# Optimization experiments

Hardware: AMD Instinct MI355X
Metric: run time of the kernel (lower is better)

Reference implementation:

```python
import jax, jax.numpy as jnp
import numpy as np
import math

B, T, C, H = 2, 2048, 1024, 16
D = C // H  # head dim = 64


def setup_inputs() -> dict:
    key = jax.random.key(0)
    ks = jax.random.split(key, 9)
    s = 1.0 / math.sqrt(C)
    inp = {
        "x": jax.random.normal(ks[0], (B, T, C), dtype=jnp.float32),
        "Wk": jax.random.normal(ks[1], (C, C), dtype=jnp.float32) * s,
        "bk": jax.random.normal(ks[2], (C,), dtype=jnp.float32) * s,
        "Wq": jax.random.normal(ks[3], (C, C), dtype=jnp.float32) * s,
        "bq": jax.random.normal(ks[4], (C,), dtype=jnp.float32) * s,
        "Wv": jax.random.normal(ks[5], (C, C), dtype=jnp.float32) * s,
        "bv": jax.random.normal(ks[6], (C,), dtype=jnp.float32) * s,
        "Wo": jax.random.normal(ks[7], (C, C), dtype=jnp.float32) * s,
        "bo": jax.random.normal(ks[8], (C,), dtype=jnp.float32) * s,
    }
    return inp


def reference(x, Wk, bk, Wq, bq, Wv, bv, Wo, bo):
    # QKV projections, split heads: [B,T,C] -> [B,H,T,D]
    def proj(W, b):
        return (x @ W.T + b).reshape(B, T, H, D).transpose(0, 2, 1, 3)

    k = proj(Wk, bk)
    q = proj(Wq, bq)
    v = proj(Wv, bv)

    # NOTE: original scales by 1/sqrt(embedding_dim), not head_dim
    scale = 1.0 / math.sqrt(C)
    scores = jnp.einsum("bhtd,bhsd->bhts", q, k) * scale  # [B,H,T,T]
    causal = jnp.tril(jnp.ones((T, T), dtype=bool))
    scores = jnp.where(causal[None, None], scores, -jnp.inf)
    attn = jax.nn.softmax(scores, axis=-1)
    y = jnp.einsum("bhts,bhsd->bhtd", attn, v)  # [B,H,T,D]
    y = y.transpose(0, 2, 1, 3).reshape(B, T, C)
    return y @ Wo.T + bo
```

## Files before the change

### kernel.cpp

```cpp
#include <hip/hip_runtime.h>
#include <hip/hip_bf16.h>
#include <stdint.h>
#include <stddef.h>

#define B_ 2
#define T_ 2048
#define C_ 1024
#define H_ 16
#define D_ 64
#define M_ (B_*T_)

typedef __attribute__((ext_vector_type(8))) short short8;
typedef __attribute__((ext_vector_type(4))) float f32x4;
typedef __attribute__((ext_vector_type(16))) float f32x16;
typedef __attribute__((ext_vector_type(4))) unsigned int u32x4;

__device__ __forceinline__ unsigned short f2bf(float f) {
    unsigned u = __float_as_uint(f);
    unsigned r = 0x7FFFu + ((u >> 16) & 1u);
    return (unsigned short)((u + r) >> 16);
}

__device__ __forceinline__ unsigned cvtpk_bf16(float lo, float hi) {
    unsigned r;
    asm("v_cvt_pk_bf16_f32 %0, %1, %2" : "=v"(r) : "v"(lo), "v"(hi));
    return r;
}

__device__ __forceinline__ float fexp2(float x) {
    float r;
    asm("v_exp_f32 %0, %1" : "=v"(r) : "v"(x));
    return r;
}

__device__ __forceinline__ void plswap(unsigned &a, unsigned &b) {
    asm("v_permlane32_swap_b32 %0, %1" : "+v"(a), "+v"(b));
}

__device__ __forceinline__ float xhalf_max(float v) {
    float a = v, b = v;
    asm("" : "+v"(b));
    asm("v_permlane32_swap_b32 %0, %1" : "+v"(a), "+v"(b));
    return fmaxf(a, b);
}
__device__ __forceinline__ float xhalf_sum(float v) {
    float a = v, b = v;
    asm("" : "+v"(b));
    asm("v_permlane32_swap_b32 %0, %1" : "+v"(a), "+v"(b));
    return a + b;
}

__device__ __forceinline__ void gload16(const void* g, void* l) {
    __builtin_amdgcn_global_load_lds(
        (__attribute__((address_space(1))) void*)g,
        (__attribute__((address_space(3))) void*)l,
        16, 0, 0);
}

__global__ void cvt_bf16(const float* __restrict__ in,
                         unsigned short* __restrict__ out, int n) {
    int idx = (blockIdx.x * blockDim.x + threadIdx.x) * 4;
    if (idx >= n) return;
    float4 v = *reinterpret_cast<const float4*>(in + idx);
    ushort4 o;
    o.x = f2bf(v.x); o.y = f2bf(v.y); o.z = f2bf(v.z); o.w = f2bf(v.w);
    *reinterpret_cast<ushort4*>(out + idx) = o;
}

__global__ void cvt_bf16_w4(const float* __restrict__ a, const float* __restrict__ b,
                            const float* __restrict__ c, const float* __restrict__ d,
                            unsigned short* __restrict__ oa, unsigned short* __restrict__ ob,
                            unsigned short* __restrict__ oc, unsigned short* __restrict__ od,
                            int n) {
    int idx = (blockIdx.x * blockDim.x + threadIdx.x) * 4;
    if (idx >= n) return;
    const float* in = (blockIdx.y == 0) ? a : (blockIdx.y == 1) ? b : (blockIdx.y == 2) ? c : d;
    unsigned short* out = (blockIdx.y == 0) ? oa : (blockIdx.y == 1) ? ob : (blockIdx.y == 2) ? oc : od;
    float4 v = *reinterpret_cast<const float4*>(in + idx);
    ushort4 o;
    o.x = f2bf(v.x); o.y = f2bf(v.y); o.z = f2bf(v.z); o.w = f2bf(v.w);
    *reinterpret_cast<ushort4*>(out + idx) = o;
}

__global__ __launch_bounds__(256) void gemm_qkv(
    const unsigned short* __restrict__ A,
    const unsigned short* __restrict__ W0,
    const unsigned short* __restrict__ W1,
    const unsigned short* __restrict__ W2,
    const float* __restrict__ b0,
    const float* __restrict__ b1,
    const float* __restrict__ b2,
    unsigned short* __restrict__ o0,
    unsigned short* __restrict__ o1,
    unsigned short* __restrict__ o2)
{
    __shared__ unsigned short As[128*32];
    __shared__ unsigned short Bs[128*32];
    int which = blockIdx.x >> 8;
    int bx = blockIdx.x & 255;
    int bm = bx >> 3, bn = bx & 7;
    const unsigned short* W = (which==0) ? W0 : ((which==1) ? W1 : W2);
    const float* bias = (which==0) ? b0 : ((which==1) ? b1 : b2);

    int tid = threadIdx.x;
    int lane = tid & 63;
    int fr = lane & 15, fq = lane >> 4;
    int wid = tid >> 6;
    int wr = wid >> 1, wc = wid & 1;

    int srow = tid >> 2;
    int scol = (tid & 3) << 3;
    const unsigned short* Ab = A + (size_t)(bm*128 + srow) * C_ + scol;
    const unsigned short* Wb = W + (size_t)(bn*128 + srow) * C_ + scol;

    f32x4 acc[4][4] = {};

    for (int kt = 0; kt < C_/32; ++kt) {
        int ko = kt*32;
        gload16(Ab + ko,            &As[tid*8]);
        gload16(Ab + 64*C_ + ko,    &As[2048 + tid*8]);
        gload16(Wb + ko,            &Bs[tid*8]);
        gload16(Wb + 64*C_ + ko,    &Bs[2048 + tid*8]);
        __syncthreads();
        short8 af[4], bfr[4];
        #pragma unroll
        for (int i = 0; i < 4; ++i) {
            af[i]  = *reinterpret_cast<const short8*>(&As[(wr*64 + i*16 + fr)*32 + fq*8]);
            bfr[i] = *reinterpret_cast<const short8*>(&Bs[(wc*64 + i*16 + fr)*32 + fq*8]);
        }
        #pragma unroll
        for (int i = 0; i < 4; ++i)
            #pragma unroll
            for (int j = 0; j < 4; ++j)
                acc[i][j] = __builtin_amdgcn_mfma_f32_16x16x32_bf16(af[i], bfr[j], acc[i][j], 0, 0, 0);
        __syncthreads();
    }

    float sc = (which == 1) ? 0.045084220f : 1.0f;
    int mbase = bm*128 + wr*64;
    int nbase = bn*128 + wc*64;
    #pragma unroll
    for (int j = 0; j < 4; ++j) {
        int col = nbase + j*16 + fr;
        float bv = bias[col];
        int h = col >> 6, d = col & 63;
        #pragma unroll
        for (int i = 0; i < 4; ++i) {
            int r0 = mbase + i*16 + fq*4;
            #pragma unroll
            for (int r = 0; r < 4; ++r) {
                float v = (acc[i][j][r] + bv) * sc;
                int m = r0 + r;
                int b = m >> 11, t = m & (T_-1);
                unsigned short hv = f2bf(v);
                if (which == 2)
                    o2[((size_t)(b*H_ + h)*D_ + d)*T_ + t] = hv;
                else {
                    unsigned short* o = (which==0) ? o0 : o1;
                    o[((size_t)(b*H_ + h)*T_ + t)*D_ + d] = hv;
                }
            }
        }
    }
}

__global__ __launch_bounds__(256) void gemm_out(
    const unsigned short* __restrict__ A,
    const unsigned short* __restrict__ W,
    const float* __restrict__ bias,
    float* __restrict__ out)
{
    __shared__ unsigned short As[128*32];
    __shared__ unsigned short Bs[128*32];
    int bx = blockIdx.x;
    int bm = bx >> 3, bn = bx & 7;

    int tid = threadIdx.x;
    int lane = tid & 63;
    int fr = lane & 15, fq = lane >> 4;
    int wid = tid >> 6;
    int wr = wid >> 1, wc = wid & 1;

    int srow = tid >> 2;
    int scol = (tid & 3) << 3;
    const unsigned short* Ab = A + (size_t)(bm*128 + srow) * C_ + scol;
    const unsigned short* Wb = W + (size_t)(bn*128 + srow) * C_ + scol;

    f32x4 acc[4][4] = {};

    for (int kt = 0; kt < C_/32; ++kt) {
        int ko = kt*32;
        gload16(Ab + ko,            &As[tid*8]);
        gload16(Ab + 64*C_ + ko,    &As[2048 + tid*8]);
        gload16(Wb + ko,            &Bs[tid*8]);
        gload16(Wb + 64*C_ + ko,    &Bs[2048 + tid*8]);
        __syncthreads();
        short8 af[4], bfr[4];
        #pragma unroll
        for (int i = 0; i < 4; ++i) {
            af[i]  = *reinterpret_cast<const short8*>(&As[(wr*64 + i*16 + fr)*32 + fq*8]);
            bfr[i] = *reinterpret_cast<const short8*>(&Bs[(wc*64 + i*16 + fr)*32 + fq*8]);
        }
        #pragma unroll
        for (int i = 0; i < 4; ++i)
            #pragma unroll
            for (int j = 0; j < 4; ++j)
                acc[i][j] = __builtin_amdgcn_mfma_f32_16x16x32_bf16(af[i], bfr[j], acc[i][j], 0, 0, 0);
        __syncthreads();
    }

    int mbase = bm*128 + wr*64;
    int nbase = bn*128 + wc*64;
    #pragma unroll
    for (int j = 0; j < 4; ++j) {
        int col = nbase + j*16 + fr;
        float bv = bias[col];
        #pragma unroll
        for (int i = 0; i < 4; ++i) {
            int r0 = mbase + i*16 + fq*4;
            #pragma unroll
            for (int r = 0; r < 4; ++r)
                out[(size_t)(r0 + r)*C_ + col] = acc[i][j][r] + bv;
        }
    }
}

__device__ __forceinline__ void attn_subtile(
    const short8 (&kf)[4], const short8 (&qf)[4],
    const short8 (&vlo)[2], const short8 (&vhi)[2],
    bool diag, int l31, int hi,
    f32x16& o0, f32x16& o1, float& m_, float& l_)
{
    f32x16 a0 = {};
    __builtin_amdgcn_s_setprio(1);
    a0 = __builtin_amdgcn_mfma_f32_32x32x16_bf16(kf[0], qf[0], a0, 0, 0, 0);
    a0 = __builtin_amdgcn_mfma_f32_32x32x16_bf16(kf[1], qf[1], a0, 0, 0, 0);
    a0 = __builtin_amdgcn_mfma_f32_32x32x16_bf16(kf[2], qf[2], a0, 0, 0, 0);
    a0 = __builtin_amdgcn_mfma_f32_32x32x16_bf16(kf[3], qf[3], a0, 0, 0, 0);
    __builtin_amdgcn_s_setprio(0);

    if (diag) {
        #pragma unroll
        for (int r = 0; r < 16; ++r) {
            int kvl = (r&3) + 8*(r>>2) + 4*hi;
            if (kvl > l31) a0[r] = -1e30f;
        }
    }

    float x0 = fmaxf(a0[0], a0[1]),   x1 = fmaxf(a0[2], a0[3]);
    float x2 = fmaxf(a0[4], a0[5]),   x3 = fmaxf(a0[6], a0[7]);
    float x4 = fmaxf(a0[8], a0[9]),   x5 = fmaxf(a0[10], a0[11]);
    float x6 = fmaxf(a0[12], a0[13]), x7 = fmaxf(a0[14], a0[15]);
    float y0 = fmaxf(x0, x1), y1 = fmaxf(x2, x3), y2 = fmaxf(x4, x5), y3 = fmaxf(x6, x7);
    float pm = fmaxf(fmaxf(y0, y1), fmaxf(y2, y3));
    pm = xhalf_max(pm);

    if (!__all(pm - m_ <= 8.0f)) {
        float mn = fmaxf(m_, pm);
        float alpha = fexp2(m_ - mn);
        l_ *= alpha;
        m_ = mn;
        #pragma unroll
        for (int r = 0; r < 16; ++r) {
            int row = (r&3) + 8*(r>>2) + 4*hi;
            float ar = __shfl(alpha, row);
            o0[r] *= ar;
            o1[r] *= ar;
        }
    }

    #pragma unroll
    for (int r = 0; r < 16; ++r)
        a0[r] = fexp2(a0[r] - m_);
    float s0 = a0[0]+a0[1],  s1 = a0[2]+a0[3],  s2 = a0[4]+a0[5],   s3 = a0[6]+a0[7];
    float s4 = a0[8]+a0[9],  s5 = a0[10]+a0[11], s6 = a0[12]+a0[13], s7 = a0[14]+a0[15];
    float u0 = s0+s1, u1 = s2+s3, u2 = s4+s5, u3 = s6+s7;
    float rs = (u0+u1) + (u2+u3);
    rs = xhalf_sum(rs);
    l_ += rs;

    unsigned pk_[8];
    #pragma unroll
    for (int jj = 0; jj < 8; ++jj)
        pk_[jj] = cvtpk_bf16(a0[2*jj], a0[2*jj+1]);

    #pragma unroll
    for (int kb = 0; kb < 2; ++kb) {
        unsigned fx = pk_[4*kb+0], fz = pk_[4*kb+2];
        unsigned fy = pk_[4*kb+1], fw = pk_[4*kb+3];
        plswap(fx, fz);
        plswap(fy, fw);
        u32x4 wv;
        wv.x = fx; wv.y = fy; wv.z = fz; wv.w = fw;
        short8 pfrag = __builtin_bit_cast(short8, wv);
        __builtin_amdgcn_s_setprio(1);
        o0 = __builtin_amdgcn_mfma_f32_32x32x16_bf16(pfrag, vlo[kb], o0, 0, 0, 0);
        o1 = __builtin_amdgcn_mfma_f32_32x32x16_bf16(pfrag, vhi[kb], o1, 0, 0, 0);
        __builtin_amdgcn_s_setprio(0);
    }
}

__global__ __launch_bounds__(256, 2) void flash_attn(
    const unsigned short* __restrict__ q,
    const unsigned short* __restrict__ k,
    const unsigned short* __restrict__ vt,
    unsigned short* __restrict__ y)
{
    __shared__ __align__(16) unsigned short ST[2][4][4096];
    float* oP  = reinterpret_cast<float*>(&ST[0][0][0]);
    float* mlP = oP + 4*32*68;

    int tid = threadIdx.x, lane = tid & 63, w = tid >> 6;
    int l31 = lane & 31, hi = lane >> 5, rsw = l31 & 7;
    int role = w >> 1, pair = w & 1;
    int bid = blockIdx.x;

    int xcd = bid & 7;
    int r = bid >> 3;
    int bh = xcd*4 + (r & 3);
    int S = 15 - (r >> 2);

    const unsigned short* kp = k  + (size_t)bh*T_*D_;
    const unsigned short* vp = vt + (size_t)bh*D_*T_;

    int rowbase = S*128 + pair*64;
    const unsigned short* qp = q + ((size_t)bh*T_ + rowbase) * D_;

    short8 qf0[4], qf1[4];
    #pragma unroll
    for (int dk = 0; dk < 4; ++dk) {
        qf0[dk] = *reinterpret_cast<const short8*>(qp + (size_t)l31*D_        + dk*16 + hi*8);
        qf1[dk] = *reinterpret_cast<const short8*>(qp + (size_t)(32 + l31)*D_ + dk*16 + hi*8);
    }

    f32x16 o00 = {}, o01 = {}, o10 = {}, o11 = {};
    float m0 = -1e30f, l0 = 0.f, m1 = -1e30f, l1 = 0.f;

    int lim0 = 4*S + 2*pair;
    int lim1 = lim0 + 1;
    int niter = S + 1;

    #define STAGE(ii, bufi)                                                            \
    {                                                                                  \
        _Pragma("unroll")                                                              \
        for (int jj = 0; jj < 2; ++jj) {                                               \
            int c2 = tid + jj*256;                                                     \
            int row_ = c2 >> 3;                                                        \
            int slot_ = (c2 & 7) ^ (row_ & 7);                                         \
            int tl_ = (ii), th_ = S + 1 + (ii);                                        \
            gload16(kp + ((size_t)(tl_*64 + row_))*D_ + slot_*8, &ST[bufi][0][c2*8]);  \
            gload16(kp + ((size_t)(th_*64 + row_))*D_ + slot_*8, &ST[bufi][1][c2*8]);  \
            gload16(vp + (size_t)row_*T_ + tl_*64 + slot_*8,     &ST[bufi][2][c2*8]);  \
            gload16(vp + (size_t)row_*T_ + th_*64 + slot_*8,     &ST[bufi][3][c2*8]);  \
        }                                                                              \
    }

    STAGE(0, 0);
    __syncthreads();

    for (int i = 0; i < niter; ++i) {
        int bufi = i & 1;
        if (i + 1 < niter) STAGE(i + 1, bufi ^ 1);

        const unsigned short* Kl = &ST[bufi][role][0];
        const unsigned short* Vl = &ST[bufi][2 + role][0];
        int t = role ? (S + 1 + i) : i;

        #pragma unroll
        for (int st = 0; st < 2; ++st) {
            int g = 2*t + st;
            if (g <= lim1) {
                short8 kf[4];
                const unsigned short* kr = Kl + (st*32 + l31)*64;
                #pragma unroll
                for (int dk = 0; dk < 4; ++dk)
                    kf[dk] = *reinterpret_cast<const short8*>(kr + (((dk<<1)|hi) ^ rsw)*8);
                short8 vlo[2], vhi[2];
                const unsigned short* vr0 = Vl + l31*64;
                const unsigned short* vr1 = Vl + (32 + l31)*64;
                #pragma unroll
                for (int kb = 0; kb < 2; ++kb) {
                    int sl = (((st<<2) | (kb<<1) | hi) ^ rsw) * 8;
                    vlo[kb] = *reinterpret_cast<const short8*>(vr0 + sl);
                    vhi[kb] = *reinterpret_cast<const short8*>(vr1 + sl);
                }
                if (g <= lim0)
                    attn_subtile(kf, qf0, vlo, vhi, g == lim0, l31, hi, o00, o01, m0, l0);
                attn_subtile(kf, qf1, vlo, vhi, g == lim1, l31, hi, o10, o11, m1, l1);
            }
        }
        __syncthreads();
    }
    #undef STAGE

    if (!role) {
        int s0 = pair*2, s1 = pair*2 + 1;
        #pragma unroll
        for (int rr = 0; rr < 16; ++rr) {
            int crow = (rr&3) + 8*(rr>>2) + 4*hi;
            oP[(s0*32 + crow)*68 + l31]      = o00[rr];
            oP[(s0*32 + crow)*68 + 32 + l31] = o01[rr];
            oP[(s1*32 + crow)*68 + l31]      = o10[rr];
            oP[(s1*32 + crow)*68 + 32 + l31] = o11[rr];
        }
        if (!hi) {
            mlP[s0*32 + l31]       = m0;
            mlP[128 + s0*32 + l31] = l0;
            mlP[s1*32 + l31]       = m1;
            mlP[128 + s1*32 + l31] = l1;
        }
    }
    __syncthreads();
    if (role) {
        int b = bh >> 4, h = bh & 15;
        #pragma unroll
        for (int qq = 0; qq < 2; ++qq) {
            int set = pair*2 + qq;
            const f32x16& po0 = qq ? o10 : o00;
            const f32x16& po1 = qq ? o11 : o01;
            float m_ = qq ? m1 : m0;
            float l_ = qq ? l1 : l0;

            float mA = mlP[set*32 + l31];
            float lA = mlP[128 + set*32 + l31];
            float mN = fmaxf(mA, m_);
            float aA = fexp2(mA - mN);
            float aB = fexp2(m_ - mN);
            float lN = lA*aA + l_*aB;
            float inv = 1.0f / lN;
            float cA = aA * inv, cB = aB * inv;

            #pragma unroll
            for (int rr = 0; rr < 16; ++rr) {
                int crow = (rr&3) + 8*(rr>>2) + 4*hi;
                float cAr = __shfl(cA, crow);
                float cBr = __shfl(cB, crow);
                float vA0 = oP[(set*32 + crow)*68 + l31];
                float vA1 = oP[(set*32 + crow)*68 + 32 + l31];
                int trow = rowbase + qq*32 + crow;
                size_t base = ((size_t)(b*T_ + trow))*C_ + h*64;
                y[base + l31]      = f2bf(vA0*cAr + po0[rr]*cBr);
                y[base + 32 + l31] = f2bf(vA1*cAr + po1[rr]*cBr);
            }
        }
    }
}

extern "C" void kernel_launch(void* const* d_in, const int* in_sizes, int n_in,
                              void* d_out, int out_size, void* d_ws, size_t ws_size,
                              hipStream_t stream) {
    const float* x  = (const float*)d_in[0];
    const float* Wk = (const float*)d_in[1];
    const float* bk = (const float*)d_in[2];
    const float* Wq = (const float*)d_in[3];
    const float* bq = (const float*)d_in[4];
    const float* Wv = (const float*)d_in[5];
    const float* bv = (const float*)d_in[6];
    const float* Wo = (const float*)d_in[7];
    const float* bo = (const float*)d_in[8];
    float* out = (float*)d_out;

    char* ws = (char*)d_ws;
    unsigned short* xb  = (unsigned short*)(ws);
    unsigned short* wkb = (unsigned short*)(ws + ((size_t)8  << 20));
    unsigned short* wqb = (unsigned short*)(ws + ((size_t)10 << 20));
    unsigned short* wvb = (unsigned short*)(ws + ((size_t)12 << 20));
    unsigned short* wob = (unsigned short*)(ws + ((size_t)14 << 20));
    unsigned short* qb  = (unsigned short*)(ws + ((size_t)16 << 20));
    unsigned short* kb  = (unsigned short*)(ws + ((size_t)24 << 20));
    unsigned short* vtb = (unsigned short*)(ws + ((size_t)32 << 20));
    unsigned short* yb  = (unsigned short*)(ws + ((size_t)40 << 20));

    const int nx = B_*T_*C_;
    const int nw = C_*C_;

    cvt_bf16<<<dim3(nx/4/256), dim3(256), 0, stream>>>(x, xb, nx);
    cvt_bf16_w4<<<dim3(nw/4/256, 4), dim3(256), 0, stream>>>(
        Wk, Wq, Wv, Wo, wkb, wqb, wvb, wob, nw);

    gemm_qkv<<<dim3(768), dim3(256), 0, stream>>>(xb, wkb, wqb, wvb, bk, bq, bv, kb, qb, vtb);

    flash_attn<<<dim3(512), dim3(256), 0, stream>>>(qb, kb, vtb, yb);

    gemm_out<<<dim3(256), dim3(256), 0, stream>>>(yb, wob, bo, out);
}
```

Measured before the change: 116.5 us.

## Double GEMM K-tile to 64 with XOR-swizzled LDS and rebalance attention block order

Both projection GEMMs now stage a 64-wide K slice per iteration instead of 32. This halves the number of barrier-separated iterations and doubles the MFMA work done between syncs. The LDS layout uses an XOR swizzle on 16-byte slots to avoid bank conflicts on the fragment reads, at the cost of doubling shared memory per block. The flash attention block-to-tile mapping also changes so the first 256 blocks take the heavy causal tiles in descending order and the second 256 take the light tiles in ascending order, aiming for better load balance.

```diff
diff --git a/kernel.cpp b/kernel.cpp
--- a/kernel.cpp
+++ b/kernel.cpp
@@ -94,8 +94,8 @@
     unsigned short* __restrict__ o1,
     unsigned short* __restrict__ o2)
 {
-    __shared__ unsigned short As[128*32];
-    __shared__ unsigned short Bs[128*32];
+    __shared__ unsigned short As[128*64];
+    __shared__ unsigned short Bs[128*64];
     int which = blockIdx.x >> 8;
     int bx = blockIdx.x & 255;
     int bm = bx >> 3, bn = bx & 7;
@@ -107,32 +107,42 @@
     int fr = lane & 15, fq = lane >> 4;
     int wid = tid >> 6;
     int wr = wid >> 1, wc = wid & 1;
-
-    int srow = tid >> 2;
-    int scol = (tid & 3) << 3;
-    const unsigned short* Ab = A + (size_t)(bm*128 + srow) * C_ + scol;
-    const unsigned short* Wb = W + (size_t)(bn*128 + srow) * C_ + scol;
+    int r7 = fr & 7;
+
+    int arow = tid >> 3;
+    int aslot = ((tid & 7) ^ (arow & 7)) << 3;
+    const unsigned short* Ab = A + (size_t)(bm*128 + arow) * C_ + aslot;
+    const unsigned short* Wb = W + (size_t)(bn*128 + arow) * C_ + aslot;
 
     f32x4 acc[4][4] = {};
 
-    for (int kt = 0; kt < C_/32; ++kt) {
-        int ko = kt*32;
-        gload16(Ab + ko,            &As[tid*8]);
-        gload16(Ab + 64*C_ + ko,    &As[2048 + tid*8]);
-        gload16(Wb + ko,            &Bs[tid*8]);
-        gload16(Wb + 64*C_ + ko,    &Bs[2048 + tid*8]);
+    for (int kt = 0; kt < C_/64; ++kt) {
+        int ko = kt*64;
+        #pragma unroll
+        for (int slab = 0; slab < 4; ++slab) {
+            gload16(Ab + (size_t)slab*32*C_ + ko, &As[slab*2048 + tid*8]);
+            gload16(Wb + (size_t)slab*32*C_ + ko, &Bs[slab*2048 + tid*8]);
+        }
         __syncthreads();
-        short8 af[4], bfr[4];
+        short8 af[4][2], bf[4][2];
         #pragma unroll
         for (int i = 0; i < 4; ++i) {
-            af[i]  = *reinterpret_cast<const short8*>(&As[(wr*64 + i*16 + fr)*32 + fq*8]);
-            bfr[i] = *reinterpret_cast<const short8*>(&Bs[(wc*64 + i*16 + fr)*32 + fq*8]);
+            int ra = (wr*64 + i*16 + fr)*64;
+            int rb = (wc*64 + i*16 + fr)*64;
+            #pragma unroll
+            for (int h = 0; h < 2; ++h) {
+                int sl = (((h<<2)|fq) ^ r7) * 8;
+                af[i][h] = *reinterpret_cast<const short8*>(&As[ra + sl]);
+                bf[i][h] = *reinterpret_cast<const short8*>(&Bs[rb + sl]);
+            }
         }
         #pragma unroll
         for (int i = 0; i < 4; ++i)
             #pragma unroll
-            for (int j = 0; j < 4; ++j)
-                acc[i][j] = __builtin_amdgcn_mfma_f32_16x16x32_bf16(af[i], bfr[j], acc[i][j], 0, 0, 0);
+            for (int j = 0; j < 4; ++j) {
+                acc[i][j] = __builtin_amdgcn_mfma_f32_16x16x32_bf16(af[i][0], bf[j][0], acc[i][j], 0, 0, 0);
+                acc[i][j] = __builtin_amdgcn_mfma_f32_16x16x32_bf16(af[i][1], bf[j][1], acc[i][j], 0, 0, 0);
+            }
         __syncthreads();
     }
 
@@ -170,8 +180,8 @@
     const float* __restrict__ bias,
     float* __restrict__ out)
 {
-    __shared__ unsigned short As[128*32];
-    __shared__ unsigned short Bs[128*32];
+    __shared__ unsigned short As[128*64];
+    __shared__ unsigned short Bs[128*64];
     int bx = blockIdx.x;
     int bm = bx >> 3, bn = bx & 7;
 
@@ -180,32 +190,42 @@
     int fr = lane & 15, fq = lane >> 4;
     int wid = tid >> 6;
     int wr = wid >> 1, wc = wid & 1;
-
-    int srow = tid >> 2;
-    int scol = (tid & 3) << 3;
-    const unsigned short* Ab = A + (size_t)(bm*128 + srow) * C_ + scol;
-    const unsigned short* Wb = W + (size_t)(bn*128 + srow) * C_ + scol;
+    int r7 = fr & 7;
+
+    int arow = tid >> 3;
+    int aslot = ((tid & 7) ^ (arow & 7)) << 3;
+    const unsigned short* Ab = A + (size_t)(bm*128 + arow) * C_ + aslot;
+    const unsigned short* Wb = W + (size_t)(bn*128 + arow) * C_ + aslot;
 
     f32x4 acc[4][4] = {};
 
-    for (int kt = 0; kt < C_/32; ++kt) {
-        int ko = kt*32;
-        gload16(Ab + ko,            &As[tid*8]);
-        gload16(Ab + 64*C_ + ko,    &As[2048 + tid*8]);
-        gload16(Wb + ko,            &Bs[tid*8]);
-        gload16(Wb + 64*C_ + ko,    &Bs[2048 + tid*8]);
+    for (int kt = 0; kt < C_/64; ++kt) {
+        int ko = kt*64;
+        #pragma unroll
+        for (int slab = 0; slab < 4; ++slab) {
+            gload16(Ab + (size_t)slab*32*C_ + ko, &As[slab*2048 + tid*8]);
+            gload16(Wb + (size_t)slab*32*C_ + ko, &Bs[slab*2048 + tid*8]);
+        }
         __syncthreads();
-        short8 af[4], bfr[4];
+        short8 af[4][2], bf[4][2];
         #pragma unroll
         for (int i = 0; i < 4; ++i) {
-            af[i]  = *reinterpret_cast<const short8*>(&As[(wr*64 + i*16 + fr)*32 + fq*8]);
-            bfr[i] = *reinterpret_cast<const short8*>(&Bs[(wc*64 + i*16 + fr)*32 + fq*8]);
+            int ra = (wr*64 + i*16 + fr)*64;
+            int rb = (wc*64 + i*16 + fr)*64;
+            #pragma unroll
+            for (int h = 0; h < 2; ++h) {
+                int sl = (((h<<2)|fq) ^ r7) * 8;
+                af[i][h] = *reinterpret_cast<const short8*>(&As[ra + sl]);
+                bf[i][h] = *reinterpret_cast<const short8*>(&Bs[rb + sl]);
+            }
         }
         #pragma unroll
         for (int i = 0; i < 4; ++i)
             #pragma unroll
-            for (int j = 0; j < 4; ++j)
-                acc[i][j] = __builtin_amdgcn_mfma_f32_16x16x32_bf16(af[i], bfr[j], acc[i][j], 0, 0, 0);
+            for (int j = 0; j < 4; ++j) {
+                acc[i][j] = __builtin_amdgcn_mfma_f32_16x16x32_bf16(af[i][0], bf[j][0], acc[i][j], 0, 0, 0);
+                acc[i][j] = __builtin_amdgcn_mfma_f32_16x16x32_bf16(af[i][1], bf[j][1], acc[i][j], 0, 0, 0);
+            }
         __syncthreads();
     }
 
@@ -315,10 +335,11 @@
     int role = w >> 1, pair = w & 1;
     int bid = blockIdx.x;
 
-    int xcd = bid & 7;
-    int r = bid >> 3;
-    int bh = xcd*4 + (r & 3);
-    int S = 15 - (r >> 2);
+    int half = bid >> 8;
+    int idx  = bid & 255;
+    int bh   = (idx & 7)*4 + ((idx >> 3) & 3);
+    int sidx = idx >> 5;
+    int S    = half ? sidx : (15 - sidx);
 
     const unsigned short* kp = k  + (size_t)bh*T_*D_;
     const unsigned short* vp = vt + (size_t)bh*D_*T_;
```

Result: slower. 130.6 us (+12.1%).
